# Kernel tuning notes

Hardware: AMD Instinct MI355X
Metric: run time of the kernel (lower is better)

The kernel has to match this reference:

```python
import jax, jax.numpy as jnp
import numpy as np

D_MODEL = 1024
NUM_HEADS = 16
DEPTH = D_MODEL // NUM_HEADS


def setup_inputs() -> dict:
    key = jax.random.key(0)
    ks = jax.random.split(key, 9)
    B, S = 2, 2048
    scale = 1.0 / np.sqrt(D_MODEL)
    x = jax.random.normal(ks[0], (B, S, D_MODEL), dtype=jnp.float32)
    wq = jax.random.normal(ks[1], (D_MODEL, D_MODEL), dtype=jnp.float32) * scale
    wk = jax.random.normal(ks[2], (D_MODEL, D_MODEL), dtype=jnp.float32) * scale
    wv = jax.random.normal(ks[3], (D_MODEL, D_MODEL), dtype=jnp.float32) * scale
    wo = jax.random.normal(ks[4], (D_MODEL, D_MODEL), dtype=jnp.float32) * scale
    bq = jnp.zeros((D_MODEL,), dtype=jnp.float32)
    bk = jnp.zeros((D_MODEL,), dtype=jnp.float32)
    bv = jnp.zeros((D_MODEL,), dtype=jnp.float32)
    bo = jnp.zeros((D_MODEL,), dtype=jnp.float32)
    return {"x": x, "wq": wq, "bq": bq, "wk": wk, "bk": bk,
            "wv": wv, "bv": bv, "wo": wo, "bo": bo}


def _split_heads(t):
    # [B, S, D] -> [B, H, S, depth]
    B, S, _ = t.shape
    return t.reshape(B, S, NUM_HEADS, DEPTH).transpose(0, 2, 1, 3)


def reference(x, wq, bq, wk, bk, wv, bv, wo, bo):
    q = _split_heads(x @ wq + bq)
    k = _split_heads(x @ wk + bk)
    v = _split_heads(x @ wv + bv)
    # scaled dot-product attention with materialized [B,H,S,S] scores
    logits = jnp.einsum("bhqd,bhkd->bhqk", q, k) / jnp.sqrt(
        jnp.asarray(DEPTH, dtype=x.dtype))
    attn = jax.nn.softmax(logits, axis=-1)
    out = jnp.einsum("bhqk,bhkd->bhqd", attn, v)
    B, _, S, _ = out.shape
    concat = out.transpose(0, 2, 1, 3).reshape(B, S, D_MODEL)
    return concat @ wo + bo
```

## Files before the change

kernel.cpp:

```cpp
#include <hip/hip_runtime.h>
#include <hip/hip_bf16.h>
#include <stdint.h>

typedef unsigned short u16;
typedef __attribute__((ext_vector_type(8))) short short8;
typedef __attribute__((ext_vector_type(4))) short s4v;
typedef __attribute__((ext_vector_type(4))) float f32x4;

__device__ __forceinline__ float bf2f(u16 u) {
    union { uint32_t u; float f; } v; v.u = ((uint32_t)u) << 16; return v.f;
}
__device__ __forceinline__ u16 f2bf(float f) {
    union { float f; uint32_t u; } v; v.f = f;
    uint32_t r = (v.u + 0x7fffu + ((v.u >> 16) & 1u)) >> 16;
    return (u16)r;
}
__device__ __forceinline__ uint32_t pkbf(float a, float b) {
    union { __hip_bfloat162 h; uint32_t w; } u;
    u.h = __float22bfloat162_rn(float2{a, b});
    return u.w;
}
__device__ __forceinline__ void store_out(u16* p, float v) { *p = f2bf(v); }
__device__ __forceinline__ void store_out(float* p, float v) { *p = v; }

__device__ __forceinline__ void async_ld16(const u16* g, u16* l) {
    __builtin_amdgcn_global_load_lds(
        (const __attribute__((address_space(1))) void*)g,
        (__attribute__((address_space(3))) void*)l, 16, 0, 0);
}

__global__ void cvt_x(const float* __restrict__ x, u16* __restrict__ xb) {
    int i = (blockIdx.x * 256 + threadIdx.x) * 8;
    float4 a = *(const float4*)(x + i);
    float4 b = *(const float4*)(x + i + 4);
    union { uint32_t w[4]; uint4 v; } o;
    o.w[0] = pkbf(a.x, a.y); o.w[1] = pkbf(a.z, a.w);
    o.w[2] = pkbf(b.x, b.y); o.w[3] = pkbf(b.z, b.w);
    *(uint4*)(xb + i) = o.v;
}

__global__ void transpose3(const float* __restrict__ w0, const float* __restrict__ w1,
                           const float* __restrict__ w2, u16* __restrict__ out) {
    const int z = blockIdx.z;
    const float* in = (z == 0) ? w0 : (z == 1) ? w1 : w2;
    u16* o = out + (size_t)z * 1024 * 1024;
    __shared__ u16 tile[32][33];
    int x = blockIdx.x * 32 + threadIdx.x;
    int y0 = blockIdx.y * 32;
#pragma unroll
    for (int j = threadIdx.y; j < 32; j += 8)
        tile[j][threadIdx.x] = f2bf(in[(size_t)(y0 + j) * 1024 + x]);
    __syncthreads();
    int ox = blockIdx.y * 32 + threadIdx.x;
    int oy0 = blockIdx.x * 32;
#pragma unroll
    for (int j = threadIdx.y; j < 32; j += 8)
        o[(size_t)(oy0 + j) * 1024 + ox] = tile[threadIdx.x][j];
}

#define GBM 128
#define GBN 128
#define GBK 32

template <typename OutT>
__global__ __launch_bounds__(256) void gemm_bt(
    const u16* __restrict__ A, int lda,
    const u16* __restrict__ BT, int ldb,
    const float* __restrict__ bias0, const float* __restrict__ bias1,
    const float* __restrict__ bias2,
    OutT* __restrict__ C, int ldc, int K) {
    __shared__ __align__(16) u16 As[GBM * GBK];
    __shared__ __align__(16) u16 Bs[GBN * GBK];

    const int tid = threadIdx.x;
    const int wave = tid >> 6, lane = tid & 63;
    const int quad = lane >> 4, l16 = lane & 15;
    const int wr = wave >> 1, wc = wave & 1;
    const int m0 = blockIdx.y * GBM, n0 = blockIdx.x * GBN;

    const int seg = n0 >> 10;
    const float* bsel = (seg == 0) ? bias0 : (seg == 1) ? bias1 : bias2;

    f32x4 acc[4][4] = {};

    const int srow = tid >> 2;
    const int scol = (tid & 3) * 8;
    const u16* Ag0 = A + (size_t)(m0 + srow) * lda + scol;
    const u16* Ag1 = Ag0 + (size_t)64 * lda;
    const u16* Bg0 = BT + (size_t)(n0 + srow) * ldb + scol;
    const u16* Bg1 = Bg0 + (size_t)64 * ldb;
    u16* As0 = As + (wave << 9);
    u16* As1 = As0 + 64 * GBK;
    u16* Bs0 = Bs + (wave << 9);
    u16* Bs1 = Bs0 + 64 * GBK;

    for (int kb = 0; kb < K; kb += GBK) {
        async_ld16(Ag0 + kb, As0);
        async_ld16(Ag1 + kb, As1);
        async_ld16(Bg0 + kb, Bs0);
        async_ld16(Bg1 + kb, Bs1);
        __syncthreads();

        short8 af[4], bf[4];
#pragma unroll
        for (int mt = 0; mt < 4; mt++)
            af[mt] = *(const short8*)(As + (wr * 64 + mt * 16 + l16) * GBK + quad * 8);
#pragma unroll
        for (int nt = 0; nt < 4; nt++)
            bf[nt] = *(const short8*)(Bs + (wc * 64 + nt * 16 + l16) * GBK + quad * 8);
#pragma unroll
        for (int mt = 0; mt < 4; mt++)
#pragma unroll
            for (int nt = 0; nt < 4; nt++)
                acc[mt][nt] = __builtin_amdgcn_mfma_f32_16x16x32_bf16(
                    af[mt], bf[nt], acc[mt][nt], 0, 0, 0);
        __syncthreads();
    }

#pragma unroll
    for (int nt = 0; nt < 4; nt++) {
        int col = n0 + wc * 64 + nt * 16 + l16;
        float bv = bsel[col & 1023];
#pragma unroll
        for (int mt = 0; mt < 4; mt++) {
            int row = m0 + wr * 64 + mt * 16 + quad * 4;
#pragma unroll
            for (int r = 0; r < 4; r++)
                store_out(&C[(size_t)(row + r) * ldc + col], acc[mt][nt][r] + bv);
        }
    }
}

#define SEQ 2048
#define BQT 128
#define BKV 128
#define LDK 72
#define LDKV 136

__global__ __launch_bounds__(256) void attn(u16* __restrict__ QKV) {
    __shared__ __align__(16) u16 Ks[BKV * LDK];
    __shared__ __align__(16) u16 Vs[64 * LDKV];

    const int tid = threadIdx.x;
    const int wave = tid >> 6, lane = tid & 63;
    const int quad = lane >> 4, l16 = lane & 15;
    const int h = blockIdx.y, bb = blockIdx.z;
    const int q0 = blockIdx.x * BQT;
    const size_t tok0 = (size_t)bb * SEQ;

    const u16* Qb = QKV + tok0 * 3072 + h * 64;
    const u16* Kb = QKV + tok0 * 3072 + 1024 + h * 64;
    const u16* Vb = QKV + tok0 * 3072 + 2048 + h * 64;

    const float cs = 0.18033688011112042f;

    int qr[2];
    qr[0] = q0 + wave * 16 + l16;
    qr[1] = qr[0] + 64;
    short8 aq[2][2];
#pragma unroll
    for (int s = 0; s < 2; s++) {
        union { short8 v; u16 u[8]; uint32_t w[4]; } qa, qb;
        qa.v = *(const short8*)(Qb + (size_t)qr[s] * 3072 + quad * 8);
        qb.v = *(const short8*)(Qb + (size_t)qr[s] * 3072 + 32 + quad * 8);
#pragma unroll
        for (int j = 0; j < 4; j++) {
            qa.w[j] = pkbf(bf2f(qa.u[2 * j]) * cs, bf2f(qa.u[2 * j + 1]) * cs);
            qb.w[j] = pkbf(bf2f(qb.u[2 * j]) * cs, bf2f(qb.u[2 * j + 1]) * cs);
        }
        aq[s][0] = qa.v; aq[s][1] = qb.v;
    }

    float l_i[2] = {0.0f, 0.0f};
    f32x4 o[2][4] = {};

    const int srow = tid >> 2;
    const int scc = (tid & 3) * 16;
    const int pr = tid & 63;
    const int dg = wave;

    const u16* kg = Kb + (size_t)srow * 3072 + scc;
    const u16* vg = Vb + (size_t)(2 * pr) * 3072 + dg * 16;

    uint4 k0r = *(const uint4*)(kg);
    uint4 k1r = *(const uint4*)(kg + 8);
    uint4 k2r = *(const uint4*)(kg + (size_t)64 * 3072);
    uint4 k3r = *(const uint4*)(kg + (size_t)64 * 3072 + 8);
    uint4 va0 = *(const uint4*)(vg);
    uint4 va1 = *(const uint4*)(vg + 8);
    uint4 vb0 = *(const uint4*)(vg + 3072);
    uint4 vb1 = *(const uint4*)(vg + 3072 + 8);

    for (int j0 = 0; j0 < SEQ; j0 += BKV) {
        *(uint4*)(Ks + srow * LDK + scc) = k0r;
        *(uint4*)(Ks + srow * LDK + scc + 8) = k1r;
        *(uint4*)(Ks + (srow + 64) * LDK + scc) = k2r;
        *(uint4*)(Ks + (srow + 64) * LDK + scc + 8) = k3r;
        {
            union { uint4 v[2]; u16 u[16]; } a, b;
            a.v[0] = va0; a.v[1] = va1; b.v[0] = vb0; b.v[1] = vb1;
#pragma unroll
            for (int j = 0; j < 16; j++) {
                uint32_t w = (uint32_t)a.u[j] | ((uint32_t)b.u[j] << 16);
                *(uint32_t*)(Vs + (dg * 16 + j) * LDKV + 2 * pr) = w;
            }
        }
        __syncthreads();

        if (j0 + BKV < SEQ) {
            size_t off = (size_t)(j0 + BKV) * 3072;
            k0r = *(const uint4*)(kg + off);
            k1r = *(const uint4*)(kg + off + 8);
            k2r = *(const uint4*)(kg + off + (size_t)64 * 3072);
            k3r = *(const uint4*)(kg + off + (size_t)64 * 3072 + 8);
            va0 = *(const uint4*)(vg + off);
            va1 = *(const uint4*)(vg + off + 8);
            vb0 = *(const uint4*)(vg + off + 3072);
            vb1 = *(const uint4*)(vg + off + 3072 + 8);
        }

        f32x4 st[2][8];
#pragma unroll
        for (int kkt = 0; kkt < 8; kkt++) {
            f32x4 s0 = {}, s1 = {};
#pragma unroll
            for (int k2 = 0; k2 < 2; k2++) {
                short8 ak = *(const short8*)(Ks + (kkt * 16 + l16) * LDK + k2 * 32 + quad * 8);
                s0 = __builtin_amdgcn_mfma_f32_16x16x32_bf16(ak, aq[0][k2], s0, 0, 0, 0);
                s1 = __builtin_amdgcn_mfma_f32_16x16x32_bf16(ak, aq[1][k2], s1, 0, 0, 0);
            }
            st[0][kkt] = s0; st[1][kkt] = s1;
        }

#pragma unroll
        for (int s = 0; s < 2; s++) {
            float ls = 0.0f;
#pragma unroll
            for (int kkt = 0; kkt < 8; kkt++)
#pragma unroll
                for (int r = 0; r < 4; r++) {
                    st[s][kkt][r] = __builtin_amdgcn_exp2f(st[s][kkt][r]);
                    ls += st[s][kkt][r];
                }
            ls += __shfl_xor(ls, 16, 64);
            ls += __shfl_xor(ls, 32, 64);
            l_i[s] += ls;
        }

#pragma unroll
        for (int kkt = 0; kkt < 8; kkt++) {
            union { uint32_t w[2]; s4v s; } bp0, bp1;
            bp0.w[0] = pkbf(st[0][kkt][0], st[0][kkt][1]);
            bp0.w[1] = pkbf(st[0][kkt][2], st[0][kkt][3]);
            bp1.w[0] = pkbf(st[1][kkt][0], st[1][kkt][1]);
            bp1.w[1] = pkbf(st[1][kkt][2], st[1][kkt][3]);
#pragma unroll
            for (int dt = 0; dt < 4; dt++) {
                s4v av = *(const s4v*)(Vs + (dt * 16 + l16) * LDKV + kkt * 16 + quad * 4);
                o[0][dt] = __builtin_amdgcn_mfma_f32_16x16x16bf16_1k(av, bp0.s, o[0][dt], 0, 0, 0);
                o[1][dt] = __builtin_amdgcn_mfma_f32_16x16x16bf16_1k(av, bp1.s, o[1][dt], 0, 0, 0);
            }
        }

        __syncthreads();
    }

#pragma unroll
    for (int s = 0; s < 2; s++) {
        const float inv_l = 1.0f / l_i[s];
        u16* orow = QKV + (tok0 + qr[s]) * 3072 + h * 64;
#pragma unroll
        for (int dt = 0; dt < 4; dt++) {
            uint32_t w0 = pkbf(o[s][dt][0] * inv_l, o[s][dt][1] * inv_l);
            uint32_t w1 = pkbf(o[s][dt][2] * inv_l, o[s][dt][3] * inv_l);
            uint2 w = {w0, w1};
            *(uint2*)(orow + dt * 16 + quad * 4) = w;
        }
    }
}

extern "C" void kernel_launch(void* const* d_in, const int* in_sizes, int n_in,
                              void* d_out, int out_size, void* d_ws, size_t ws_size,
                              hipStream_t stream) {
    const float* x  = (const float*)d_in[0];
    const float* wq = (const float*)d_in[1];
    const float* bq = (const float*)d_in[2];
    const float* wk = (const float*)d_in[3];
    const float* bk = (const float*)d_in[4];
    const float* wv = (const float*)d_in[5];
    const float* bv = (const float*)d_in[6];
    const float* wo = (const float*)d_in[7];
    const float* bo = (const float*)d_in[8];
    (void)in_sizes; (void)n_in; (void)out_size; (void)ws_size;

    u16* QKV = (u16*)d_ws;
    u16* wT  = QKV + (size_t)4096 * 3072;
    u16* xb  = wT + (size_t)3 * 1024 * 1024;
    u16* woT = xb;

    cvt_x<<<dim3(2048), dim3(256), 0, stream>>>(x, xb);
    transpose3<<<dim3(32, 32, 3), dim3(32, 8), 0, stream>>>(wq, wk, wv, wT);
    gemm_bt<u16><<<dim3(24, 32), 256, 0, stream>>>(xb, 1024, wT, 1024, bq, bk, bv,
                                                   QKV, 3072, 1024);
    transpose3<<<dim3(32, 32, 1), dim3(32, 8), 0, stream>>>(wo, wo, wo, woT);
    attn<<<dim3(16, 16, 2), 256, 0, stream>>>(QKV);
    gemm_bt<float><<<dim3(8, 32), 256, 0, stream>>>(QKV, 3072, woT, 1024, bo, bo, bo,
                                                    (float*)d_out, 1024, 1024);
}
```

Baseline: 214.5 us.

## Split attention KV range across two blocks and add combine kernel

The attention grid is doubled so that each block processes only half of the key/value sequence. Each block writes an unnormalized partial output and its softmax denominator, and a new combine kernel sums the two partials and normalizes. This relies on the softmax having no running-max rescaling, so the partial sums simply add. The aim is more blocks to fill the CUs, at the cost of an extra kernel launch and extra global traffic. There is a race risk: the second-half blocks write their partial into the Q region that first-half blocks read.

```diff
diff --git a/kernel.cpp b/kernel.cpp
--- a/kernel.cpp
+++ b/kernel.cpp
@@ -137,16 +137,20 @@
 #define LDK 72
 #define LDKV 136
 
-__global__ __launch_bounds__(256) void attn(u16* __restrict__ QKV) {
+__global__ __launch_bounds__(256) void attn(u16* __restrict__ QKV,
+                                            u16* __restrict__ Opart,
+                                            float* __restrict__ lpart) {
     __shared__ __align__(16) u16 Ks[BKV * LDK];
     __shared__ __align__(16) u16 Vs[64 * LDKV];
 
     const int tid = threadIdx.x;
     const int wave = tid >> 6, lane = tid & 63;
     const int quad = lane >> 4, l16 = lane & 15;
-    const int h = blockIdx.y, bb = blockIdx.z;
+    const int h = blockIdx.y;
+    const int bb = blockIdx.z & 1, half = blockIdx.z >> 1;
     const int q0 = blockIdx.x * BQT;
     const size_t tok0 = (size_t)bb * SEQ;
+    const int kv0 = half * (SEQ / 2);
 
     const u16* Qb = QKV + tok0 * 3072 + h * 64;
     const u16* Kb = QKV + tok0 * 3072 + 1024 + h * 64;
@@ -179,8 +183,8 @@
     const int pr = tid & 63;
     const int dg = wave;
 
-    const u16* kg = Kb + (size_t)srow * 3072 + scc;
-    const u16* vg = Vb + (size_t)(2 * pr) * 3072 + dg * 16;
+    const u16* kg = Kb + (size_t)(kv0 + srow) * 3072 + scc;
+    const u16* vg = Vb + (size_t)(kv0 + 2 * pr) * 3072 + dg * 16;
 
     uint4 k0r = *(const uint4*)(kg);
     uint4 k1r = *(const uint4*)(kg + 8);
@@ -191,7 +195,7 @@
     uint4 vb0 = *(const uint4*)(vg + 3072);
     uint4 vb1 = *(const uint4*)(vg + 3072 + 8);
 
-    for (int j0 = 0; j0 < SEQ; j0 += BKV) {
+    for (int j0 = 0; j0 < SEQ / 2; j0 += BKV) {
         *(uint4*)(Ks + srow * LDK + scc) = k0r;
         *(uint4*)(Ks + srow * LDK + scc + 8) = k1r;
         *(uint4*)(Ks + (srow + 64) * LDK + scc) = k2r;
@@ -207,7 +211,7 @@
         }
         __syncthreads();
 
-        if (j0 + BKV < SEQ) {
+        if (j0 + BKV < SEQ / 2) {
             size_t off = (size_t)(j0 + BKV) * 3072;
             k0r = *(const uint4*)(kg + off);
             k1r = *(const uint4*)(kg + off + 8);
@@ -267,16 +271,40 @@
 
 #pragma unroll
     for (int s = 0; s < 2; s++) {
-        const float inv_l = 1.0f / l_i[s];
-        u16* orow = QKV + (tok0 + qr[s]) * 3072 + h * 64;
+        u16* obase = half ? (QKV + (tok0 + qr[s]) * 3072 + h * 64)
+                          : (Opart + (tok0 + qr[s]) * 1024 + h * 64);
 #pragma unroll
         for (int dt = 0; dt < 4; dt++) {
-            uint32_t w0 = pkbf(o[s][dt][0] * inv_l, o[s][dt][1] * inv_l);
-            uint32_t w1 = pkbf(o[s][dt][2] * inv_l, o[s][dt][3] * inv_l);
+            uint32_t w0 = pkbf(o[s][dt][0], o[s][dt][1]);
+            uint32_t w1 = pkbf(o[s][dt][2], o[s][dt][3]);
             uint2 w = {w0, w1};
-            *(uint2*)(orow + dt * 16 + quad * 4) = w;
-        }
-    }
+            *(uint2*)(obase + dt * 16 + quad * 4) = w;
+        }
+        if (quad == 0)
+            lpart[(size_t)half * 4096 * 16 + (tok0 + qr[s]) * 16 + h] = l_i[s];
+    }
+}
+
+__global__ __launch_bounds__(256) void combine(u16* __restrict__ QKV,
+                                               const u16* __restrict__ Opart,
+                                               const float* __restrict__ lpart) {
+    int gid = blockIdx.x * 256 + threadIdx.x;
+    int t = gid >> 7;
+    int c8 = (gid & 127) * 8;
+    int h = c8 >> 6;
+    float l0 = lpart[(size_t)t * 16 + h];
+    float l1 = lpart[(size_t)4096 * 16 + (size_t)t * 16 + h];
+    float inv = 1.0f / (l0 + l1);
+    union { uint4 v; u16 u[8]; } a, b, o;
+    a.v = *(const uint4*)(Opart + (size_t)t * 1024 + c8);
+    u16* qp = QKV + (size_t)t * 3072 + c8;
+    b.v = *(const uint4*)(qp);
+    union { uint32_t w[4]; uint4 v; } ov;
+#pragma unroll
+    for (int j = 0; j < 4; j++)
+        ov.w[j] = pkbf((bf2f(a.u[2 * j]) + bf2f(b.u[2 * j])) * inv,
+                       (bf2f(a.u[2 * j + 1]) + bf2f(b.u[2 * j + 1])) * inv);
+    *(uint4*)(qp) = ov.v;
 }
 
 extern "C" void kernel_launch(void* const* d_in, const int* in_sizes, int n_in,
@@ -296,14 +324,17 @@
     u16* QKV = (u16*)d_ws;
     u16* wT  = QKV + (size_t)4096 * 3072;
     u16* xb  = wT + (size_t)3 * 1024 * 1024;
-    u16* woT = xb;
+    u16* Opart = wT;
+    float* lpart = (float*)(Opart + (size_t)4096 * 1024);
+    u16* woT = xb + (size_t)3 * 1024 * 1024;
 
     cvt_x<<<dim3(2048), dim3(256), 0, stream>>>(x, xb);
     transpose3<<<dim3(32, 32, 3), dim3(32, 8), 0, stream>>>(wq, wk, wv, wT);
     gemm_bt<u16><<<dim3(24, 32), 256, 0, stream>>>(xb, 1024, wT, 1024, bq, bk, bv,
                                                    QKV, 3072, 1024);
     transpose3<<<dim3(32, 32, 1), dim3(32, 8), 0, stream>>>(wo, wo, wo, woT);
-    attn<<<dim3(16, 16, 2), 256, 0, stream>>>(QKV);
+    attn<<<dim3(16, 16, 4), 256, 0, stream>>>(QKV, Opart, lpart);
+    combine<<<dim3(2048), dim3(256), 0, stream>>>(QKV, Opart, lpart);
     gemm_bt<float><<<dim3(8, 32), 256, 0, stream>>>(QKV, 3072, woT, 1024, bo, bo, bo,
                                                     (float*)d_out, 1024, 1024);
 }
```

New measurement: 224.6 us. 4.7% more time.
